# Kernel optimization log

Measured on AMD Instinct MI355X. Metric: run time of the kernel, lower is better.

The kernel has to match this reference:

```python
import jax, jax.numpy as jnp
import numpy as np

N_NODES = 50000
N_EDGES = 800000
IN_DIM = 128
HID = 8
HEADS = 8
OUT_DIM = 64
NEG_SLOPE = 0.2


def setup_inputs() -> dict:
    key = jax.random.key(0)
    ks = jax.random.split(key, 8)
    x = jax.random.normal(ks[0], (N_NODES, IN_DIM), dtype=jnp.float32)
    edge_index = jax.random.randint(ks[1], (2, N_EDGES), 0, N_NODES, dtype=jnp.int64)
    W1 = jax.random.normal(ks[2], (IN_DIM, HEADS * HID), dtype=jnp.float32) / np.sqrt(IN_DIM)
    a_src1 = jax.random.normal(ks[3], (HEADS, HID), dtype=jnp.float32)
    a_dst1 = jax.random.normal(ks[4], (HEADS, HID), dtype=jnp.float32)
    b1 = jnp.zeros((HEADS * HID,), dtype=jnp.float32)
    W2 = jax.random.normal(ks[5], (HEADS * HID, OUT_DIM), dtype=jnp.float32) / np.sqrt(HEADS * HID)
    a_src2 = jax.random.normal(ks[6], (1, OUT_DIM), dtype=jnp.float32)
    a_dst2 = jax.random.normal(ks[7], (1, OUT_DIM), dtype=jnp.float32)
    b2 = jnp.zeros((OUT_DIM,), dtype=jnp.float32)
    return {"x": x, "edge_index": edge_index, "W1": W1, "a_src1": a_src1,
            "a_dst1": a_dst1, "b1": b1, "W2": W2, "a_src2": a_src2,
            "a_dst2": a_dst2, "b2": b2}


def gat_conv(x, src, dst, W, a_src, a_dst, b, heads, ch):
    # PyG GATConv (eval mode): linear -> per-edge LeakyReLU score ->
    # segment-softmax over incoming edges -> weighted scatter-add -> +bias
    n = x.shape[0]
    h = (x @ W).reshape(n, heads, ch)               # [N,H,C]
    score_src = jnp.einsum('nhc,hc->nh', h, a_src)  # [N,H]
    score_dst = jnp.einsum('nhc,hc->nh', h, a_dst)  # [N,H]
    e = jax.nn.leaky_relu(score_src[src] + score_dst[dst], NEG_SLOPE)  # [E,H]
    m = jax.ops.segment_max(e, dst, num_segments=n)
    m = jnp.where(jnp.isfinite(m), m, 0.0)
    p = jnp.exp(e - m[dst])
    denom = jax.ops.segment_sum(p, dst, num_segments=n)
    alpha = p / (denom[dst] + 1e-16)                # [E,H]
    out = jax.ops.segment_sum(h[src] * alpha[:, :, None], dst, num_segments=n)
    return out.reshape(n, heads * ch) + b


def reference(x, edge_index, W1, a_src1, a_dst1, b1, W2, a_src2, a_dst2, b2):
    n = x.shape[0]
    # add_self_loops=True (PyG default)
    loops = jnp.arange(n, dtype=edge_index.dtype)
    src = jnp.concatenate([edge_index[0], loops])
    dst = jnp.concatenate([edge_index[1], loops])
    h = gat_conv(x, src, dst, W1, a_src1, a_dst1, b1, HEADS, HID)
    h = jax.nn.elu(h)
    out = gat_conv(h, src, dst, W2, a_src2, a_dst2, b2, 1, OUT_DIM)
    return out
```

## Files before the change

kernel.cpp:

```cpp
#include <hip/hip_runtime.h>
#include <hip/hip_fp16.h>
#include <math.h>
#include <stdint.h>

#define N_NODES 50000
#define N_EDGES 800000
#define ET (N_EDGES + N_NODES)
#define IN_DIM 128
#define H1DIM 64
#define HEADS 8
#define HID 8
#define OUT_DIM 64
#define NEG_SLOPE 0.2f

#define NB ((N_NODES + 255) / 256)
#define CAP 5120
#define RC2 4

#define LIN1_WAVES (N_NODES / 16)
#define LIN1_BLOCKS ((LIN1_WAVES + 3) / 4)

#define EPT 8
#define HB ((N_EDGES + 256*EPT - 1) / (256*EPT))

typedef _Float16 half8 __attribute__((ext_vector_type(8)));
typedef float f32x4 __attribute__((ext_vector_type(4)));

__device__ __forceinline__ float lrelu(float v) { return v >= 0.f ? v : NEG_SLOPE * v; }

__device__ __forceinline__ void fma8raw(uint4 u, float alpha, float* a) {
    float2 f0 = __half22float2(*(const __half2*)&u.x);
    float2 f1 = __half22float2(*(const __half2*)&u.y);
    float2 f2 = __half22float2(*(const __half2*)&u.z);
    float2 f3 = __half22float2(*(const __half2*)&u.w);
    a[0] += f0.x * alpha; a[1] += f0.y * alpha;
    a[2] += f1.x * alpha; a[3] += f1.y * alpha;
    a[4] += f2.x * alpha; a[5] += f2.y * alpha;
    a[6] += f3.x * alpha; a[7] += f3.y * alpha;
}

__device__ __forceinline__ void fma8h(const __half* __restrict__ base, float alpha, float* a) {
    fma8raw(*reinterpret_cast<const uint4*>(base), alpha, a);
}


__global__ __launch_bounds__(256) void prep_kernel(
    const float* __restrict__ W1, const float* __restrict__ W2,
    __half* __restrict__ w1fH, __half* __restrict__ w1fL,
    __half* __restrict__ w2fH, __half* __restrict__ w2fL,
    int* __restrict__ cursor)
{
    int b = blockIdx.x;
    if (b < 32) {
        int idx = b * 256 + threadIdx.x;
        int f = idx >> 9, rr = idx & 511;
        int l = rr >> 3, j = rr & 7;
        int ks = f >> 2, ct = f & 3;
        int k = ks * 32 + ((l >> 4) << 3) + j;
        int c = (ct << 4) + (l & 15);
        float w = W1[k * 64 + c];
        __half hi = __float2half(w);
        w1fH[idx] = hi;
        w1fL[idx] = __float2half(w - __half2float(hi));
    } else if (b < 48) {
        int idx = (b - 32) * 256 + threadIdx.x;
        int f = idx >> 9, rr = idx & 511;
        int l = rr >> 3, j = rr & 7;
        int ks = f >> 2, ct = f & 3;
        int k = ks * 32 + ((l >> 4) << 3) + j;
        int c = (ct << 4) + (l & 15);
        float w = W2[k * 64 + c];
        __half hi = __float2half(w);
        w2fH[idx] = hi;
        w2fL[idx] = __float2half(w - __half2float(hi));
    } else {
        for (int k = threadIdx.x; k < 16 * NB; k += 256) cursor[k] = 0;
    }
}


__global__ __launch_bounds__(256) void cl1_kernel(
    const int* __restrict__ ei, int* __restrict__ cursor, int* __restrict__ ebuf,
    const float* __restrict__ x,
    const __half* __restrict__ w1fH, const __half* __restrict__ w1fL,
    const float* __restrict__ a_src, const float* __restrict__ a_dst,
    __half* __restrict__ h1, float* __restrict__ ssrc, float* __restrict__ sdst)
{
    __shared__ int hist[NB];
    __shared__ int res[NB];
    if (blockIdx.x < HB) {
        for (int k = threadIdx.x; k < NB; k += 256) hist[k] = 0;
        __syncthreads();
        int base = blockIdx.x * (256 * EPT) + threadIdx.x;
        int ss[EPT], ds[EPT];
        #pragma unroll
        for (int j = 0; j < EPT; ++j) {
            int e = base + j * 256;
            ds[j] = -1;
            if (e < N_EDGES) {
                ss[j] = ei[e];
                ds[j] = ei[N_EDGES + e];
                atomicAdd(&hist[ds[j] >> 8], 1);
            }
        }
        __syncthreads();
        if (threadIdx.x < NB) {
            int h = hist[threadIdx.x];
            res[threadIdx.x] = h ? atomicAdd(&cursor[threadIdx.x * 16], h) : 0;
            hist[threadIdx.x] = 0;
        }
        __syncthreads();
        #pragma unroll
        for (int j = 0; j < EPT; ++j) {
            if (ds[j] >= 0) {
                int b = ds[j] >> 8;
                int r = atomicAdd(&hist[b], 1);
                int idx = res[b] + r;
                if (idx < CAP) ebuf[b * CAP + idx] = ss[j] | ((ds[j] & 255) << 16);
            }
        }
        return;
    }

    int wid = threadIdx.x >> 6, t = threadIdx.x & 63;
    int g = (blockIdx.x - HB) * 4 + wid;
    if (g >= LIN1_WAVES) return;
    int n0 = g * 16;
    int row = t & 15, kq = t >> 4;

    f32x4 acc[4] = {};
    const float* xp = x + (size_t)(n0 + row) * IN_DIM + kq * 8;
    #pragma unroll
    for (int ks = 0; ks < 4; ++ks) {
        float4 u0 = *reinterpret_cast<const float4*>(xp + ks * 32);
        float4 u1 = *reinterpret_cast<const float4*>(xp + ks * 32 + 4);
        float xv[8] = {u0.x, u0.y, u0.z, u0.w, u1.x, u1.y, u1.z, u1.w};
        half8 ah, al;
        #pragma unroll
        for (int j = 0; j < 8; ++j) {
            _Float16 h = (_Float16)xv[j];
            ah[j] = h;
            al[j] = (_Float16)(xv[j] - (float)h);
        }
        #pragma unroll
        for (int ct = 0; ct < 4; ++ct) {
            int f = ks * 4 + ct;
            half8 bh = *reinterpret_cast<const half8*>(w1fH + f * 512 + t * 8);
            half8 bl = *reinterpret_cast<const half8*>(w1fL + f * 512 + t * 8);
            acc[ct] = __builtin_amdgcn_mfma_f32_16x16x32_f16(ah, bh, acc[ct], 0, 0, 0);
            acc[ct] = __builtin_amdgcn_mfma_f32_16x16x32_f16(al, bh, acc[ct], 0, 0, 0);
            acc[ct] = __builtin_amdgcn_mfma_f32_16x16x32_f16(ah, bl, acc[ct], 0, 0, 0);
        }
    }

    float asv[4], adv[4];
    #pragma unroll
    for (int ct = 0; ct < 4; ++ct) {
        asv[ct] = a_src[ct * 16 + (t & 15)];
        adv[ct] = a_dst[ct * 16 + (t & 15)];
    }
    int rbase = n0 + (t >> 4) * 4;
    #pragma unroll
    for (int r = 0; r < 4; ++r) {
        int n = rbase + r;
        #pragma unroll
        for (int ct = 0; ct < 4; ++ct) {
            float v = acc[ct][r];
            h1[(size_t)n * 64 + ct * 16 + (t & 15)] = __float2half(v);
            float ps = v * asv[ct], pd = v * adv[ct];
            ps += __shfl_xor(ps, 1); ps += __shfl_xor(ps, 2); ps += __shfl_xor(ps, 4);
            pd += __shfl_xor(pd, 1); pd += __shfl_xor(pd, 2); pd += __shfl_xor(pd, 4);
            if ((t & 7) == 0) {
                int hd = ct * 2 + ((t >> 3) & 1);
                ssrc[n * 8 + hd] = ps;
                sdst[n * 8 + hd] = pd;
            }
        }
    }
}


__global__ __launch_bounds__(512) void p2_kernel(
    const int* __restrict__ cursor, const int* __restrict__ ebuf,
    int* __restrict__ rowp, int* __restrict__ adj)
{
    __shared__ int sb[256];
    __shared__ int cnt[256];
    __shared__ int sh[256];
    __shared__ int cur[256];
    int b = blockIdx.x, t = threadIdx.x;

    if (t < 256) sb[t] = (t < NB) ? cursor[t * 16] : 0;
    __syncthreads();
    #pragma unroll
    for (int o = 1; o < 256; o <<= 1) {
        int add = (t < 256 && t >= o) ? sb[t - o] : 0;
        __syncthreads();
        if (t < 256) sb[t] += add;
        __syncthreads();
    }
    int m = cursor[b * 16];
    int eb0 = sb[b] - m;

    int n0 = b * 256;
    int nn = N_NODES - n0; if (nn > 256) nn = 256;
    if (t < 256) cnt[t] = (t < nn) ? 1 : 0;
    __syncthreads();
    const int* eb = ebuf + b * CAP;
    for (int e = t; e < m; e += 512)
        atomicAdd(&cnt[eb[e] >> 16], 1);
    __syncthreads();
    int myc = (t < 256) ? cnt[t] : 0;
    if (t < 256) sh[t] = myc;
    __syncthreads();
    #pragma unroll
    for (int o = 1; o < 256; o <<= 1) {
        int add = (t < 256 && t >= o) ? sh[t - o] : 0;
        __syncthreads();
        if (t < 256) sh[t] += add;
        __syncthreads();
    }
    int ab = eb0 + n0;
    if (t < 256) {
        int myoff = ab + sh[t] - myc;
        cur[t] = myoff;
        if (t < nn) rowp[n0 + t] = myoff;
        if (b == 0 && t == 0) rowp[N_NODES] = ET;
    }
    __syncthreads();
    for (int e = t; e < m; e += 512) {
        int v = eb[e];
        int r = atomicAdd(&cur[v >> 16], 1);
        adj[r] = v & 0xFFFF;
    }
}

__global__ __launch_bounds__(256) void p2b_kernel(
    const int* __restrict__ rowp, int* __restrict__ adj)
{
    int n = blockIdx.x * 256 + threadIdx.x;
    if (n < N_NODES) adj[rowp[n + 1] - 1] = n;
}


__global__ __launch_bounds__(256) void l1_kernel(
    const int* __restrict__ row, const int* __restrict__ adj,
    const __half* __restrict__ h1, const float* __restrict__ s1, const float* __restrict__ t1,
    const float* __restrict__ b1, __half* __restrict__ ha)
{
    int wid = threadIdx.x >> 6, t = threadIdx.x & 63;
    int n = blockIdx.x * 4 + wid;
    int beg = row[n], end = row[n + 1];
    int slot = t >> 3, h = t & 7;
    float sd = t1[n * 8 + h];
    const int e0 = beg + slot;

    float p[RC2];
    uint4 raw[RC2];
    float m = -3e38f;
    #pragma unroll
    for (int it = 0; it < RC2; ++it) {
        int e = e0 + it * 8;
        bool ok = e < end;
        int s = ok ? adj[e] : n;
        float v = ok ? lrelu(s1[s * 8 + h] + sd) : -3e38f;
        p[it] = v;
        m = fmaxf(m, v);
        raw[it] = *reinterpret_cast<const uint4*>(h1 + (size_t)s * 64 + h * 8);
    }
    for (int e = e0 + RC2 * 8; e < end; e += 8)
        m = fmaxf(m, lrelu(s1[adj[e] * 8 + h] + sd));
    m = fmaxf(m, __shfl_xor(m, 8));
    m = fmaxf(m, __shfl_xor(m, 16));
    m = fmaxf(m, __shfl_xor(m, 32));

    float den = 0.f;
    #pragma unroll
    for (int it = 0; it < RC2; ++it) {
        float pe = __expf(p[it] - m);
        p[it] = pe;
        den += pe;
    }
    for (int e = e0 + RC2 * 8; e < end; e += 8)
        den += __expf(lrelu(s1[adj[e] * 8 + h] + sd) - m);
    den += __shfl_xor(den, 8);
    den += __shfl_xor(den, 16);
    den += __shfl_xor(den, 32);
    float inv = 1.f / (den + 1e-16f);

    float a[8] = {0,0,0,0,0,0,0,0};
    #pragma unroll
    for (int it = 0; it < RC2; ++it) fma8raw(raw[it], p[it] * inv, a);
    for (int e = e0 + RC2 * 8; e < end; e += 8) {
        int s = adj[e];
        float alpha = __expf(lrelu(s1[s * 8 + h] + sd) - m) * inv;
        fma8h(h1 + (size_t)s * 64 + h * 8, alpha, a);
    }
    #pragma unroll
    for (int j = 0; j < 8; ++j) {
        a[j] += __shfl_xor(a[j], 8);
        a[j] += __shfl_xor(a[j], 16);
        a[j] += __shfl_xor(a[j], 32);
    }

    if (slot < 4) {
        int j0 = slot * 2;
        float v0 = a[j0]     + b1[h * 8 + j0];
        float v1 = a[j0 + 1] + b1[h * 8 + j0 + 1];
        v0 = v0 > 0.f ? v0 : (__expf(v0) - 1.f);
        v1 = v1 > 0.f ? v1 : (__expf(v1) - 1.f);
        __half2 hv;
        hv.x = __float2half(v0);
        hv.y = __float2half(v1);
        *reinterpret_cast<__half2*>(ha + (size_t)n * 64 + h * 8 + j0) = hv;
    }
}


__global__ __launch_bounds__(256) void lin2_kernel(
    const __half* __restrict__ ha,
    const __half* __restrict__ w2fH, const __half* __restrict__ w2fL,
    const float* __restrict__ as2, const float* __restrict__ ad2,
    __half* __restrict__ h2, float* __restrict__ s2, float* __restrict__ t2)
{
    int tid = threadIdx.x;
    int wid = tid >> 6, t = tid & 63;
    int g = blockIdx.x * 4 + wid;
    if (g >= LIN1_WAVES) return;
    int n0 = g * 16;
    int row = t & 15, kq = t >> 4;

    f32x4 acc[4] = {};
    const __half* xp = ha + (size_t)(n0 + row) * 64 + kq * 8;
    #pragma unroll
    for (int ks = 0; ks < 2; ++ks) {
        half8 ahv = *reinterpret_cast<const half8*>(xp + ks * 32);
        #pragma unroll
        for (int ct = 0; ct < 4; ++ct) {
            int f = ks * 4 + ct;
            half8 bh = *reinterpret_cast<const half8*>(w2fH + f * 512 + t * 8);
            half8 bl = *reinterpret_cast<const half8*>(w2fL + f * 512 + t * 8);
            acc[ct] = __builtin_amdgcn_mfma_f32_16x16x32_f16(ahv, bh, acc[ct], 0, 0, 0);
            acc[ct] = __builtin_amdgcn_mfma_f32_16x16x32_f16(ahv, bl, acc[ct], 0, 0, 0);
        }
    }

    float asv[4], adv[4];
    #pragma unroll
    for (int ct = 0; ct < 4; ++ct) {
        asv[ct] = as2[ct * 16 + (t & 15)];
        adv[ct] = ad2[ct * 16 + (t & 15)];
    }
    int rbase = n0 + (t >> 4) * 4;
    #pragma unroll
    for (int r = 0; r < 4; ++r) {
        int n = rbase + r;
        float ps = 0.f, pd = 0.f;
        #pragma unroll
        for (int ct = 0; ct < 4; ++ct) {
            float v = acc[ct][r];
            h2[(size_t)n * 64 + ct * 16 + (t & 15)] = __float2half(v);
            ps += v * asv[ct];
            pd += v * adv[ct];
        }
        ps += __shfl_xor(ps, 1); ps += __shfl_xor(ps, 2);
        ps += __shfl_xor(ps, 4); ps += __shfl_xor(ps, 8);
        pd += __shfl_xor(pd, 1); pd += __shfl_xor(pd, 2);
        pd += __shfl_xor(pd, 4); pd += __shfl_xor(pd, 8);
        if ((t & 15) == 0) { s2[n] = ps; t2[n] = pd; }
    }
}


__global__ __launch_bounds__(256) void l2_kernel(
    const int* __restrict__ row, const int* __restrict__ adj,
    const __half* __restrict__ h2, const float* __restrict__ s2, const float* __restrict__ t2,
    const float* __restrict__ b2, float* __restrict__ out)
{
    int wid = threadIdx.x >> 6, t = threadIdx.x & 63;
    int n = blockIdx.x * 4 + wid;
    int beg = row[n], end = row[n + 1];
    int slot = t >> 3, g = t & 7;
    float sd = t2[n];
    const int e0 = beg + slot;

    float p[RC2];
    uint4 raw[RC2];
    float m = -3e38f;
    #pragma unroll
    for (int it = 0; it < RC2; ++it) {
        int e = e0 + it * 8;
        bool ok = e < end;
        int s = ok ? adj[e] : n;
        float v = ok ? lrelu(s2[s] + sd) : -3e38f;
        p[it] = v;
        m = fmaxf(m, v);
        raw[it] = *reinterpret_cast<const uint4*>(h2 + (size_t)s * 64 + g * 8);
    }
    for (int e = e0 + RC2 * 8; e < end; e += 8)
        m = fmaxf(m, lrelu(s2[adj[e]] + sd));
    m = fmaxf(m, __shfl_xor(m, 8));
    m = fmaxf(m, __shfl_xor(m, 16));
    m = fmaxf(m, __shfl_xor(m, 32));

    float den = 0.f;
    #pragma unroll
    for (int it = 0; it < RC2; ++it) {
        float pe = __expf(p[it] - m);
        p[it] = pe;
        den += pe;
    }
    for (int e = e0 + RC2 * 8; e < end; e += 8)
        den += __expf(lrelu(s2[adj[e]] + sd) - m);
    den += __shfl_xor(den, 8);
    den += __shfl_xor(den, 16);
    den += __shfl_xor(den, 32);
    float inv = 1.f / (den + 1e-16f);

    float a[8] = {0,0,0,0,0,0,0,0};
    #pragma unroll
    for (int it = 0; it < RC2; ++it) fma8raw(raw[it], p[it] * inv, a);
    for (int e = e0 + RC2 * 8; e < end; e += 8) {
        int s = adj[e];
        float alpha = __expf(lrelu(s2[s] + sd) - m) * inv;
        fma8h(h2 + (size_t)s * 64 + g * 8, alpha, a);
    }
    #pragma unroll
    for (int j = 0; j < 8; ++j) {
        a[j] += __shfl_xor(a[j], 8);
        a[j] += __shfl_xor(a[j], 16);
        a[j] += __shfl_xor(a[j], 32);
    }
    if (slot == 0) {
        float4 o0 = make_float4(a[0] + b2[g * 8 + 0], a[1] + b2[g * 8 + 1],
                                a[2] + b2[g * 8 + 2], a[3] + b2[g * 8 + 3]);
        float4 o1 = make_float4(a[4] + b2[g * 8 + 4], a[5] + b2[g * 8 + 5],
                                a[6] + b2[g * 8 + 6], a[7] + b2[g * 8 + 7]);
        float4* op = (float4*)(out + (size_t)n * 64 + g * 8);
        op[0] = o0; op[1] = o1;
    }
}

extern "C" void kernel_launch(void* const* d_in, const int* in_sizes, int n_in,
                              void* d_out, int out_size, void* d_ws, size_t ws_size,
                              hipStream_t stream)
{
    const float* x   = (const float*)d_in[0];
    const int* ei    = (const int*)d_in[1];
    const float* W1  = (const float*)d_in[2];
    const float* as1 = (const float*)d_in[3];
    const float* ad1 = (const float*)d_in[4];
    const float* b1  = (const float*)d_in[5];
    const float* W2  = (const float*)d_in[6];
    const float* as2 = (const float*)d_in[7];
    const float* ad2 = (const float*)d_in[8];
    const float* b2  = (const float*)d_in[9];
    float* out = (float*)d_out;

    char* wsb = (char*)d_ws;
    __half* h1   = (__half*)wsb;
    __half* h2   = h1 + (size_t)N_NODES * 64;
    __half* ha   = h2 + (size_t)N_NODES * 64;
    __half* w1fH = ha + (size_t)N_NODES * 64;
    __half* w1fL = w1fH + 8192;
    __half* w2fH = w1fL + 8192;
    __half* w2fL = w2fH + 4096;
    float*  s1   = (float*)(w2fL + 4096);
    float*  t1   = s1 + N_NODES * 8;
    float*  s2   = t1 + N_NODES * 8;
    float*  t2   = s2 + N_NODES;
    int*    cursor = (int*)(t2 + N_NODES);
    int*    rowp   = cursor + 16 * NB;
    int*    adj    = rowp + N_NODES + 1;
    int*    ebuf   = adj + ET;

    prep_kernel<<<49, 256, 0, stream>>>(W1, W2, w1fH, w1fL, w2fH, w2fL, cursor);

    cl1_kernel<<<HB + LIN1_BLOCKS, 256, 0, stream>>>(ei, cursor, ebuf, x, w1fH, w1fL,
                                                     as1, ad1, h1, s1, t1);

    p2_kernel<<<NB, 512, 0, stream>>>(cursor, ebuf, rowp, adj);
    p2b_kernel<<<(N_NODES + 255) / 256, 256, 0, stream>>>(rowp, adj);

    l1_kernel<<<N_NODES / 4, 256, 0, stream>>>(rowp, adj, h1, s1, t1, b1, ha);

    lin2_kernel<<<LIN1_BLOCKS, 256, 0, stream>>>(ha, w2fH, w2fL, as2, ad2, h2, s2, t2);

    l2_kernel<<<N_NODES / 4, 256, 0, stream>>>(rowp, adj, h2, s2, t2, b2, out);
}
```

Measured before the change: 190.0 us.

## Fuse layer-2 linear into layer-1 aggregation and handle self-loops implicitly

Self-loop edges are no longer stored in the CSR adjacency. The aggregation loops extend to e<=end and substitute the node itself, which removes the p2b kernel and shrinks adj. The layer-2 linear transform and its attention scores are folded into the layer-1 aggregation kernel: each wave applies ELU, then computes a 64-wide fp32 matvec with W2 via shuffles. This drops the ha intermediate buffer, the lin2 MFMA kernel and the W2 split-precision prep, at the cost of a per-node scalar matvec in the aggregation kernel and an extra self-loop iteration per lane group.

Measured after the change: 208.1 us. +9.6%, slower.

```diff
diff --git a/kernel.cpp b/kernel.cpp
--- a/kernel.cpp
+++ b/kernel.cpp
@@ -5,7 +5,6 @@
 
 #define N_NODES 50000
 #define N_EDGES 800000
-#define ET (N_EDGES + N_NODES)
 #define IN_DIM 128
 #define H1DIM 64
 #define HEADS 8
@@ -45,9 +44,8 @@
 
 
 __global__ __launch_bounds__(256) void prep_kernel(
-    const float* __restrict__ W1, const float* __restrict__ W2,
+    const float* __restrict__ W1,
     __half* __restrict__ w1fH, __half* __restrict__ w1fL,
-    __half* __restrict__ w2fH, __half* __restrict__ w2fL,
     int* __restrict__ cursor)
 {
     int b = blockIdx.x;
@@ -62,17 +60,6 @@
         __half hi = __float2half(w);
         w1fH[idx] = hi;
         w1fL[idx] = __float2half(w - __half2float(hi));
-    } else if (b < 48) {
-        int idx = (b - 32) * 256 + threadIdx.x;
-        int f = idx >> 9, rr = idx & 511;
-        int l = rr >> 3, j = rr & 7;
-        int ks = f >> 2, ct = f & 3;
-        int k = ks * 32 + ((l >> 4) << 3) + j;
-        int c = (ct << 4) + (l & 15);
-        float w = W2[k * 64 + c];
-        __half hi = __float2half(w);
-        w2fH[idx] = hi;
-        w2fL[idx] = __float2half(w - __half2float(hi));
     } else {
         for (int k = threadIdx.x; k < 16 * NB; k += 256) cursor[k] = 0;
     }
@@ -190,7 +177,10 @@
     __shared__ int cur[256];
     int b = blockIdx.x, t = threadIdx.x;
 
-    if (t < 256) sb[t] = (t < NB) ? cursor[t * 16] : 0;
+    if (t < 256) {
+        int c = (t < NB) ? cursor[t * 16] : 0;
+        sb[t] = c < CAP ? c : CAP;
+    }
     __syncthreads();
     #pragma unroll
     for (int o = 1; o < 256; o <<= 1) {
@@ -199,12 +189,12 @@
         if (t < 256) sb[t] += add;
         __syncthreads();
     }
-    int m = cursor[b * 16];
+    int m = cursor[b * 16]; if (m > CAP) m = CAP;
     int eb0 = sb[b] - m;
 
     int n0 = b * 256;
     int nn = N_NODES - n0; if (nn > 256) nn = 256;
-    if (t < 256) cnt[t] = (t < nn) ? 1 : 0;
+    if (t < 256) cnt[t] = 0;
     __syncthreads();
     const int* eb = ebuf + b * CAP;
     for (int e = t; e < m; e += 512)
@@ -220,12 +210,11 @@
         if (t < 256) sh[t] += add;
         __syncthreads();
     }
-    int ab = eb0 + n0;
     if (t < 256) {
-        int myoff = ab + sh[t] - myc;
+        int myoff = eb0 + sh[t] - myc;
         cur[t] = myoff;
         if (t < nn) rowp[n0 + t] = myoff;
-        if (b == 0 && t == 0) rowp[N_NODES] = ET;
+        if (b == 0 && t == 0) rowp[N_NODES] = N_EDGES;
     }
     __syncthreads();
     for (int e = t; e < m; e += 512) {
@@ -235,18 +224,13 @@
     }
 }
 
-__global__ __launch_bounds__(256) void p2b_kernel(
-    const int* __restrict__ rowp, int* __restrict__ adj)
-{
-    int n = blockIdx.x * 256 + threadIdx.x;
-    if (n < N_NODES) adj[rowp[n + 1] - 1] = n;
-}
-
-
-__global__ __launch_bounds__(256) void l1_kernel(
+
+__global__ __launch_bounds__(256) void l1x_kernel(
     const int* __restrict__ row, const int* __restrict__ adj,
     const __half* __restrict__ h1, const float* __restrict__ s1, const float* __restrict__ t1,
-    const float* __restrict__ b1, __half* __restrict__ ha)
+    const float* __restrict__ b1, const float* __restrict__ W2,
+    const float* __restrict__ as2, const float* __restrict__ ad2,
+    __half* __restrict__ h2, float* __restrict__ s2, float* __restrict__ t2)
 {
     int wid = threadIdx.x >> 6, t = threadIdx.x & 63;
     int n = blockIdx.x * 4 + wid;
@@ -261,15 +245,16 @@
     #pragma unroll
     for (int it = 0; it < RC2; ++it) {
         int e = e0 + it * 8;
-        bool ok = e < end;
-        int s = ok ? adj[e] : n;
-        float v = ok ? lrelu(s1[s * 8 + h] + sd) : -3e38f;
+        int s = (e < end) ? adj[e] : n;
+        float v = (e <= end) ? lrelu(s1[s * 8 + h] + sd) : -3e38f;
         p[it] = v;
         m = fmaxf(m, v);
         raw[it] = *reinterpret_cast<const uint4*>(h1 + (size_t)s * 64 + h * 8);
     }
-    for (int e = e0 + RC2 * 8; e < end; e += 8)
-        m = fmaxf(m, lrelu(s1[adj[e] * 8 + h] + sd));
+    for (int e = e0 + RC2 * 8; e <= end; e += 8) {
+        int s = (e < end) ? adj[e] : n;
+        m = fmaxf(m, lrelu(s1[s * 8 + h] + sd));
+    }
     m = fmaxf(m, __shfl_xor(m, 8));
     m = fmaxf(m, __shfl_xor(m, 16));
     m = fmaxf(m, __shfl_xor(m, 32));
@@ -281,8 +266,10 @@
         p[it] = pe;
         den += pe;
     }
-    for (int e = e0 + RC2 * 8; e < end; e += 8)
-        den += __expf(lrelu(s1[adj[e] * 8 + h] + sd) - m);
+    for (int e = e0 + RC2 * 8; e <= end; e += 8) {
+        int s = (e < end) ? adj[e] : n;
+        den += __expf(lrelu(s1[s * 8 + h] + sd) - m);
+    }
     den += __shfl_xor(den, 8);
     den += __shfl_xor(den, 16);
     den += __shfl_xor(den, 32);
@@ -291,8 +278,8 @@
     float a[8] = {0,0,0,0,0,0,0,0};
     #pragma unroll
     for (int it = 0; it < RC2; ++it) fma8raw(raw[it], p[it] * inv, a);
-    for (int e = e0 + RC2 * 8; e < end; e += 8) {
-        int s = adj[e];
+    for (int e = e0 + RC2 * 8; e <= end; e += 8) {
+        int s = (e < end) ? adj[e] : n;
         float alpha = __expf(lrelu(s1[s * 8 + h] + sd) - m) * inv;
         fma8h(h1 + (size_t)s * 64 + h * 8, alpha, a);
     }
@@ -303,72 +290,29 @@
         a[j] += __shfl_xor(a[j], 32);
     }
 
-    if (slot < 4) {
-        int j0 = slot * 2;
-        float v0 = a[j0]     + b1[h * 8 + j0];
-        float v1 = a[j0 + 1] + b1[h * 8 + j0 + 1];
-        v0 = v0 > 0.f ? v0 : (__expf(v0) - 1.f);
-        v1 = v1 > 0.f ? v1 : (__expf(v1) - 1.f);
-        __half2 hv;
-        hv.x = __float2half(v0);
-        hv.y = __float2half(v1);
-        *reinterpret_cast<__half2*>(ha + (size_t)n * 64 + h * 8 + j0) = hv;
-    }
-}
-
-
-__global__ __launch_bounds__(256) void lin2_kernel(
-    const __half* __restrict__ ha,
-    const __half* __restrict__ w2fH, const __half* __restrict__ w2fL,
-    const float* __restrict__ as2, const float* __restrict__ ad2,
-    __half* __restrict__ h2, float* __restrict__ s2, float* __restrict__ t2)
-{
-    int tid = threadIdx.x;
-    int wid = tid >> 6, t = tid & 63;
-    int g = blockIdx.x * 4 + wid;
-    if (g >= LIN1_WAVES) return;
-    int n0 = g * 16;
-    int row = t & 15, kq = t >> 4;
-
-    f32x4 acc[4] = {};
-    const __half* xp = ha + (size_t)(n0 + row) * 64 + kq * 8;
-    #pragma unroll
-    for (int ks = 0; ks < 2; ++ks) {
-        half8 ahv = *reinterpret_cast<const half8*>(xp + ks * 32);
-        #pragma unroll
-        for (int ct = 0; ct < 4; ++ct) {
-            int f = ks * 4 + ct;
-            half8 bh = *reinterpret_cast<const half8*>(w2fH + f * 512 + t * 8);
-            half8 bl = *reinterpret_cast<const half8*>(w2fL + f * 512 + t * 8);
-            acc[ct] = __builtin_amdgcn_mfma_f32_16x16x32_f16(ahv, bh, acc[ct], 0, 0, 0);
-            acc[ct] = __builtin_amdgcn_mfma_f32_16x16x32_f16(ahv, bl, acc[ct], 0, 0, 0);
-        }
-    }
-
-    float asv[4], adv[4];
-    #pragma unroll
-    for (int ct = 0; ct < 4; ++ct) {
-        asv[ct] = as2[ct * 16 + (t & 15)];
-        adv[ct] = ad2[ct * 16 + (t & 15)];
-    }
-    int rbase = n0 + (t >> 4) * 4;
-    #pragma unroll
-    for (int r = 0; r < 4; ++r) {
-        int n = rbase + r;
-        float ps = 0.f, pd = 0.f;
-        #pragma unroll
-        for (int ct = 0; ct < 4; ++ct) {
-            float v = acc[ct][r];
-            h2[(size_t)n * 64 + ct * 16 + (t & 15)] = __float2half(v);
-            ps += v * asv[ct];
-            pd += v * adv[ct];
-        }
-        ps += __shfl_xor(ps, 1); ps += __shfl_xor(ps, 2);
-        ps += __shfl_xor(ps, 4); ps += __shfl_xor(ps, 8);
-        pd += __shfl_xor(pd, 1); pd += __shfl_xor(pd, 2);
-        pd += __shfl_xor(pd, 4); pd += __shfl_xor(pd, 8);
-        if ((t & 15) == 0) { s2[n] = ps; t2[n] = pd; }
-    }
+    float ae[8];
+    #pragma unroll
+    for (int j = 0; j < 8; ++j) {
+        float v = a[j] + b1[h * 8 + j];
+        ae[j] = v > 0.f ? v : (__expf(v) - 1.f);
+    }
+
+    float c0 = 0.f;
+    #pragma unroll 8
+    for (int k = 0; k < 64; ++k) {
+        float hk = __shfl(ae[k & 7], k >> 3);
+        c0 += hk * W2[k * 64 + t];
+    }
+    h2[(size_t)n * 64 + t] = __float2half(c0);
+
+    float rs = c0 * as2[t];
+    float rd = c0 * ad2[t];
+    #pragma unroll
+    for (int mk = 32; mk >= 1; mk >>= 1) {
+        rs += __shfl_xor(rs, mk);
+        rd += __shfl_xor(rd, mk);
+    }
+    if (t == 0) { s2[n] = rs; t2[n] = rd; }
 }
 
 
@@ -390,15 +334,16 @@
     #pragma unroll
     for (int it = 0; it < RC2; ++it) {
         int e = e0 + it * 8;
-        bool ok = e < end;
-        int s = ok ? adj[e] : n;
-        float v = ok ? lrelu(s2[s] + sd) : -3e38f;
+        int s = (e < end) ? adj[e] : n;
+        float v = (e <= end) ? lrelu(s2[s] + sd) : -3e38f;
         p[it] = v;
         m = fmaxf(m, v);
         raw[it] = *reinterpret_cast<const uint4*>(h2 + (size_t)s * 64 + g * 8);
     }
-    for (int e = e0 + RC2 * 8; e < end; e += 8)
-        m = fmaxf(m, lrelu(s2[adj[e]] + sd));
+    for (int e = e0 + RC2 * 8; e <= end; e += 8) {
+        int s = (e < end) ? adj[e] : n;
+        m = fmaxf(m, lrelu(s2[s] + sd));
+    }
     m = fmaxf(m, __shfl_xor(m, 8));
     m = fmaxf(m, __shfl_xor(m, 16));
     m = fmaxf(m, __shfl_xor(m, 32));
@@ -410,8 +355,10 @@
         p[it] = pe;
         den += pe;
     }
-    for (int e = e0 + RC2 * 8; e < end; e += 8)
-        den += __expf(lrelu(s2[adj[e]] + sd) - m);
+    for (int e = e0 + RC2 * 8; e <= end; e += 8) {
+        int s = (e < end) ? adj[e] : n;
+        den += __expf(lrelu(s2[s] + sd) - m);
+    }
     den += __shfl_xor(den, 8);
     den += __shfl_xor(den, 16);
     den += __shfl_xor(den, 32);
@@ -420,8 +367,8 @@
     float a[8] = {0,0,0,0,0,0,0,0};
     #pragma unroll
     for (int it = 0; it < RC2; ++it) fma8raw(raw[it], p[it] * inv, a);
-    for (int e = e0 + RC2 * 8; e < end; e += 8) {
-        int s = adj[e];
+    for (int e = e0 + RC2 * 8; e <= end; e += 8) {
+        int s = (e < end) ? adj[e] : n;
         float alpha = __expf(lrelu(s2[s] + sd) - m) * inv;
         fma8h(h2 + (size_t)s * 64 + g * 8, alpha, a);
     }
@@ -460,31 +407,26 @@
     char* wsb = (char*)d_ws;
     __half* h1   = (__half*)wsb;
     __half* h2   = h1 + (size_t)N_NODES * 64;
-    __half* ha   = h2 + (size_t)N_NODES * 64;
-    __half* w1fH = ha + (size_t)N_NODES * 64;
+    __half* w1fH = h2 + (size_t)N_NODES * 64;
     __half* w1fL = w1fH + 8192;
-    __half* w2fH = w1fL + 8192;
-    __half* w2fL = w2fH + 4096;
-    float*  s1   = (float*)(w2fL + 4096);
+    float*  s1   = (float*)(w1fL + 8192);
     float*  t1   = s1 + N_NODES * 8;
     float*  s2   = t1 + N_NODES * 8;
     float*  t2   = s2 + N_NODES;
     int*    cursor = (int*)(t2 + N_NODES);
     int*    rowp   = cursor + 16 * NB;
     int*    adj    = rowp + N_NODES + 1;
-    int*    ebuf   = adj + ET;
-
-    prep_kernel<<<49, 256, 0, stream>>>(W1, W2, w1fH, w1fL, w2fH, w2fL, cursor);
+    int*    ebuf   = adj + N_EDGES;
+
+    prep_kernel<<<33, 256, 0, stream>>>(W1, w1fH, w1fL, cursor);
 
     cl1_kernel<<<HB + LIN1_BLOCKS, 256, 0, stream>>>(ei, cursor, ebuf, x, w1fH, w1fL,
                                                      as1, ad1, h1, s1, t1);
 
     p2_kernel<<<NB, 512, 0, stream>>>(cursor, ebuf, rowp, adj);
-    p2b_kernel<<<(N_NODES + 255) / 256, 256, 0, stream>>>(rowp, adj);
-
-    l1_kernel<<<N_NODES / 4, 256, 0, stream>>>(rowp, adj, h1, s1, t1, b1, ha);
-
-    lin2_kernel<<<LIN1_BLOCKS, 256, 0, stream>>>(ha, w2fH, w2fL, as2, ad2, h2, s2, t2);
+
+    l1x_kernel<<<N_NODES / 4, 256, 0, stream>>>(rowp, adj, h1, s1, t1, b1,
+                                                W2, as2, ad2, h2, s2, t2);
 
     l2_kernel<<<N_NODES / 4, 256, 0, stream>>>(rowp, adj, h2, s2, t2, b2, out);
 }
```
